# Optimization experiments

Measured on AMD Instinct MI355X. Metric: run time of the kernel, lower is better.

Reference implementation:

```python
import jax, jax.numpy as jnp
import numpy as np
from jax.scipy.special import logsumexp

L = 15      # DATA_MAX_SEG_LEN
K = 64      # XCRIBE_DIM
H = 16      # SEG_DIM
TAG = 32    # TAG_DIM
DUR = 4     # DURATION_DIM
NY = 15     # len(LABELS)
N = 16384   # sequence length
S = 2048    # number of gold segments
NEG = jnp.float32(-1e30)


def setup_inputs() -> dict:
    key = jax.random.key(0)
    ks = jax.random.split(key, 24)
    sL = 1.0 / np.sqrt(H)
    sV = 1.0 / np.sqrt(2 * H + TAG + DUR)
    sW = 1.0 / np.sqrt(H)

    def U(k, shape, s):
        return jax.random.uniform(k, shape, jnp.float32, -s, s)

    return dict(
        data=jax.random.normal(ks[0], (N, K), jnp.float32),
        fwd_Wih=U(ks[1], (4 * H, K), sL), fwd_Whh=U(ks[2], (4 * H, H), sL),
        fwd_bih=U(ks[3], (4 * H,), sL), fwd_bhh=U(ks[4], (4 * H,), sL),
        bwd_Wih=U(ks[5], (4 * H, K), sL), bwd_Whh=U(ks[6], (4 * H, H), sL),
        bwd_bih=U(ks[7], (4 * H,), sL), bwd_bhh=U(ks[8], (4 * H,), sL),
        fwd_h0=jax.random.normal(ks[9], (H,), jnp.float32),
        fwd_c0=jax.random.normal(ks[10], (H,), jnp.float32),
        bwd_h0=jax.random.normal(ks[11], (H,), jnp.float32),
        bwd_c0=jax.random.normal(ks[12], (H,), jnp.float32),
        Y_enc=jax.random.normal(ks[13], (NY, TAG), jnp.float32),
        Z_enc=jax.random.normal(ks[14], (L, DUR), jnp.float32),
        V_W=U(ks[15], (H, 2 * H + TAG + DUR), sV), V_b=U(ks[16], (H,), sV),
        W_W=U(ks[17], (1, H), sW), W_b=U(ks[18], (1,), sW),
        tags=jax.random.randint(ks[19], (S,), 0, NY),
        lengths=jax.random.randint(ks[20], (S,), 1, L + 1),
    )


def _lstm(xs, Wih, Whh, bih, bhh, h0, c0):
    # xs: [L, B, K] -> hidden outputs [L, B, H]; torch gate order i,f,g,o
    B = xs.shape[1]
    b = bih + bhh

    def step(carry, x):
        h, c = carry
        g = x @ Wih.T + h @ Whh.T + b
        i, f, gg, o = jnp.split(g, 4, axis=-1)
        c = jax.nn.sigmoid(f) * c + jax.nn.sigmoid(i) * jnp.tanh(gg)
        h = jax.nn.sigmoid(o) * jnp.tanh(c)
        return (h, c), h

    init = (jnp.broadcast_to(h0, (B, H)), jnp.broadcast_to(c0, (B, H)))
    _, hs = jax.lax.scan(step, init, xs)
    return hs


def reference(data, fwd_Wih, fwd_Whh, fwd_bih, fwd_bhh, fwd_h0, fwd_c0,
              bwd_Wih, bwd_Whh, bwd_bih, bwd_bhh, bwd_h0, bwd_c0,
              Y_enc, Z_enc, V_W, V_b, W_W, W_b, tags, lengths):
    n = data.shape[0]
    pos = jnp.arange(n)[:, None]      # [N,1]
    dd = jnp.arange(L)[None, :]       # [1,L]
    idx_f = jnp.minimum(pos + dd, n - 1)   # forward window indices
    idx_b = pos - dd                       # backward window indices (may be <0)

    win_f = data[idx_f].transpose(1, 0, 2)                  # [L,N,K]
    win_b = data[jnp.maximum(idx_b, 0)].transpose(1, 0, 2)  # [L,N,K]

    # fwd[i,d] = forward_precalc[i][i+d]; bwd[e,d] = backward_precalc[e-d][e]
    fwd = _lstm(win_f, fwd_Wih, fwd_Whh, fwd_bih, fwd_bhh, fwd_h0, fwd_c0).transpose(1, 0, 2)
    bwd = _lstm(win_b, bwd_Wih, bwd_Whh, bwd_bih, bwd_bhh, bwd_h0, bwd_c0).transpose(1, 0, 2)

    # gather fwd at (start=e-d, duration index d) -> aligned with end position e
    fwd_g = fwd[jnp.maximum(idx_b, 0), dd]          # [N,L,H]
    fb = jnp.concatenate([fwd_g, bwd], axis=-1)     # [N,L,2H]

    # split V across concat blocks: [fwd,bwd | Y | Z]
    V1 = V_W[:, :2 * H]; V2 = V_W[:, 2 * H:2 * H + TAG]; V3 = V_W[:, 2 * H + TAG:]
    base = fb @ V1.T + (Z_enc @ V3.T)[None, :, :] + V_b      # [N,L,H]
    ypart = Y_enc @ V2.T                                     # [NY,H]
    pre = base[:, :, None, :] + ypart[None, None, :, :]      # [N,L,NY,H]
    scores = jnp.tanh(pre) @ W_W[0] + W_b[0]                 # [N,L,NY]

    valid = idx_b >= 0
    A = jnp.where(valid, logsumexp(scores, axis=-1), NEG)    # [N,L] lse over labels

    # semi-Markov forward DP: log_alpha[i] = lse_d(log_alpha[i-d] + A[i-1,d-1])
    def dp(hist, a):  # hist[k] = log_alpha[i-1-k]
        new = logsumexp(hist + a)
        return jnp.concatenate([new[None], hist[:-1]]), new

    hist0 = jnp.full((L,), NEG, jnp.float32).at[0].set(0.0)
    _, alphas = jax.lax.scan(dp, hist0, A)
    logZ = alphas[-1]

    # gold-segment score; original never advances `chars`, so start is always 0
    gv = lengths < L
    gscores = scores[lengths - 1, lengths - 1, tags]
    indiv = jnp.sum(jnp.where(gv, gscores, 0.0))
    return logZ - indiv
```

## Files before the change

### kernel.cpp

```cpp
#include <hip/hip_runtime.h>

#define NPOS 16384
#define NEG  (-1e30f)

#define OFF_FWDH  0
#define OFF_BWDH  1966080
#define OFF_T0    4194304
#define OFF_R     4251904
#define OFF_IND   4255776

struct Params {
    const float *data, *fWih, *fWhh, *fbih, *fbhh, *bWih, *bWhh, *bbih, *bbhh;
    const float *h0f, *c0f, *h0b, *c0b, *Yenc, *Zenc, *VW, *Vb, *WW, *Wb;
    const int *tags, *lengths;
    float *ws; float *out;
};

typedef _Float16 half2_t __attribute__((ext_vector_type(2)));

__device__ __forceinline__ half2_t u2h(unsigned int v) {
    return __builtin_bit_cast(half2_t, v);
}
__device__ __forceinline__ unsigned int packh(float a, float b) {
    half2_t h = { (_Float16)a, (_Float16)b };
    return __builtin_bit_cast(unsigned int, h);
}
__device__ __forceinline__ float fdot2_(unsigned int w, unsigned int x, float acc) {
    return __builtin_amdgcn_fdot2(u2h(w), u2h(x), acc, false);
}
__device__ __forceinline__ float sigf(float x) {
    return __builtin_amdgcn_rcpf(1.0f + __expf(-x));
}
__device__ __forceinline__ float tanhf_(float x) {
    return 1.0f - 2.0f * __builtin_amdgcn_rcpf(1.0f + __expf(2.0f * x));
}
__device__ __forceinline__ float lse15(const float* tv) {
    float a0 = fmaxf(tv[0], tv[1]),  a1 = fmaxf(tv[2], tv[3]);
    float a2 = fmaxf(tv[4], tv[5]),  a3 = fmaxf(tv[6], tv[7]);
    float a4 = fmaxf(tv[8], tv[9]),  a5 = fmaxf(tv[10], tv[11]);
    float a6 = fmaxf(tv[12], tv[13]);
    float b0 = fmaxf(a0, a1), b1 = fmaxf(a2, a3), b2 = fmaxf(a4, a5), b3 = fmaxf(a6, tv[14]);
    float mx = fmaxf(fmaxf(b0, b1), fmaxf(b2, b3));
    float e[15];
    #pragma unroll
    for (int i = 0; i < 15; i++) e[i] = __expf(tv[i] - mx);
    float s0 = e[0]+e[1], s1 = e[2]+e[3], s2 = e[4]+e[5], s3 = e[6]+e[7];
    float s4 = e[8]+e[9], s5 = e[10]+e[11], s6 = e[12]+e[13];
    float t0 = s0+s1, t1 = s2+s3, t2 = s4+s5, t3 = s6+e[14];
    return mx + __logf((t0+t1) + (t2+t3));
}

__device__ __forceinline__ void lse_mm(const float* src, float* dst, int nprod,
                                       int tid, int nthr)
{
    const int tot = nprod * 225;
    for (int e = tid; e < tot; e += nthr) {
        const int m = e / 225;
        const int r = e - m * 225;
        const int i = r / 15;
        const int j = r - i * 15;
        const float* Ar = src + (2*m + 1)*240 + i*16;
        const float* Bc = src + (2*m)*240 + j;
        float tv[15];
        #pragma unroll
        for (int k = 0; k < 15; k++) tv[k] = Ar[k] + Bc[k*16];
        dst[m*240 + i*16 + j] = lse15(tv);
    }
}

__global__ __launch_bounds__(512) void kA(Params p)
{
    __shared__ unsigned int xs2[78*33];
    __shared__ float xgT[64*78];
    __shared__ unsigned int hsh[2*512];
    __shared__ unsigned int wqx[2048];
    __shared__ unsigned int wqh[512];
    __shared__ float bq[64];

    const int tid  = threadIdx.x;
    const int lane = tid & 63;
    const int wq   = __builtin_amdgcn_readfirstlane(tid >> 6);
    const int dir  = blockIdx.y;
    const int P0   = blockIdx.x << 6;
    const int dbase = P0 - (dir ? 14 : 0);

    const float* Wih = dir ? p.bWih : p.fWih;
    const float* Whh = dir ? p.bWhh : p.fWhh;
    const float* bih = dir ? p.bbih : p.fbih;
    const float* bhh = dir ? p.bbhh : p.fbhh;
    const float* h0  = dir ? p.h0b  : p.h0f;
    const float* c0  = dir ? p.c0b  : p.c0f;

    for (int e = tid; e < 2048; e += 512) {
        int k2 = e >> 6, pi = e & 63;
        int w = pi >> 3, jj = pi & 7;
        int j = ((jj >> 1) << 4) + 2*w + (jj & 1);
        wqx[e] = packh(Wih[j*64 + 2*k2], Wih[j*64 + 2*k2 + 1]);
    }
    if (tid < 512) {
        int m2 = tid >> 6, pi = tid & 63;
        int w = pi >> 3, jj = pi & 7;
        int j = ((jj >> 1) << 4) + 2*w + (jj & 1);
        wqh[tid] = packh(Whh[j*16 + 2*m2], Whh[j*16 + 2*m2 + 1]);
    }
    if (tid < 64) {
        int w = tid >> 3, jj = tid & 7;
        int j = ((jj >> 1) << 4) + 2*w + (jj & 1);
        bq[tid] = bih[j] + bhh[j];
    }
    for (int idx = tid; idx < 78*32; idx += 512) {
        int r = idx >> 5, c = idx & 31;
        int q = dbase + r;
        q = q < 0 ? 0 : (q > NPOS-1 ? NPOS-1 : q);
        float2 x2 = *(const float2*)(p.data + (size_t)q*64 + c*2);
        xs2[r*33 + c] = packh(x2.x, x2.y);
    }
    if (tid < 512) {
        int m2 = tid >> 6;
        hsh[tid] = packh(h0[2*m2], h0[2*m2 + 1]);
    }
    __syncthreads();

    {
        float acc[8];
        #pragma unroll
        for (int jj = 0; jj < 8; jj++) acc[jj] = bq[wq*8 + jj];
        #pragma unroll 8
        for (int k2 = 0; k2 < 32; k2++) {
            unsigned int xp = xs2[lane*33 + k2];
            uint4 w0 = *(const uint4*)&wqx[k2*64 + wq*8];
            uint4 w1 = *(const uint4*)&wqx[k2*64 + wq*8 + 4];
            acc[0] = fdot2_(w0.x, xp, acc[0]);
            acc[1] = fdot2_(w0.y, xp, acc[1]);
            acc[2] = fdot2_(w0.z, xp, acc[2]);
            acc[3] = fdot2_(w0.w, xp, acc[3]);
            acc[4] = fdot2_(w1.x, xp, acc[4]);
            acc[5] = fdot2_(w1.y, xp, acc[5]);
            acc[6] = fdot2_(w1.z, xp, acc[6]);
            acc[7] = fdot2_(w1.w, xp, acc[7]);
        }
        #pragma unroll
        for (int jj = 0; jj < 8; jj++) xgT[(wq*8 + jj)*78 + lane] = acc[jj];
    }
    #pragma unroll
    for (int it = 0; it < 2; it++) {
        int e = tid + it*512;
        if (e < 896) {
            int rw = 64 + (e >> 6);
            int g  = e & 63;
            float acc = bq[g];
            #pragma unroll 8
            for (int k2 = 0; k2 < 32; k2++)
                acc = fdot2_(wqx[k2*64 + g], xs2[rw*33 + k2], acc);
            xgT[g*78 + rw] = acc;
        }
    }
    float cv0 = c0[wq*2], cv1 = c0[wq*2 + 1];
    unsigned int* outH = (unsigned int*)(p.ws + (dir ? OFF_BWDH : OFF_FWDH));
    __syncthreads();

    int buf = 0;
    for (int d = 0; d < 15; d++) {
        const int row = dir ? (lane + 14 - d) : (lane + d);
        float part[8];
        #pragma unroll
        for (int jj = 0; jj < 8; jj++) part[jj] = xgT[(wq*8 + jj)*78 + row];
        #pragma unroll
        for (int m2 = 0; m2 < 8; m2++) {
            unsigned int hp = hsh[buf*512 + m2*64 + lane];
            uint4 w0 = *(const uint4*)&wqh[m2*64 + wq*8];
            uint4 w1 = *(const uint4*)&wqh[m2*64 + wq*8 + 4];
            part[0] = fdot2_(w0.x, hp, part[0]);
            part[1] = fdot2_(w0.y, hp, part[1]);
            part[2] = fdot2_(w0.z, hp, part[2]);
            part[3] = fdot2_(w0.w, hp, part[3]);
            part[4] = fdot2_(w1.x, hp, part[4]);
            part[5] = fdot2_(w1.y, hp, part[5]);
            part[6] = fdot2_(w1.z, hp, part[6]);
            part[7] = fdot2_(w1.w, hp, part[7]);
        }
        float cn0 = sigf(part[2])*cv0 + sigf(part[0])*tanhf_(part[4]);
        float cn1 = sigf(part[3])*cv1 + sigf(part[1])*tanhf_(part[5]);
        cv0 = cn0; cv1 = cn1;
        float h0v = sigf(part[6])*tanhf_(cn0);
        float h1v = sigf(part[7])*tanhf_(cn1);
        unsigned int pk = packh(h0v, h1v);
        hsh[(buf^1)*512 + wq*64 + lane] = pk;
        outH[((size_t)d*NPOS + P0 + lane)*8 + wq] = pk;
        __syncthreads();
        buf ^= 1;
    }
}

__global__ __launch_bounds__(1024) void kBC(Params p)
{
    __shared__ float As[64*17];
    __shared__ unsigned int VWh[256];
    __shared__ float zbl[240];
    __shared__ float EY[240];
    __shared__ float Ms[16*240];
    __shared__ float Mp[8*240];
    __shared__ float gscL[240];
    __shared__ float red[16];
    const int tid = threadIdx.x;
    const int P0  = blockIdx.x << 6;
    float* ws = p.ws;

    if (tid < 240) {
        int y = tid >> 4, h = tid & 15;
        const float4* Y4 = (const float4*)(p.Yenc + y*32);
        const float4* V4 = (const float4*)(p.VW + h*68 + 32);
        float acc = 0.f;
        #pragma unroll
        for (int t = 0; t < 8; t++) {
            float4 a = Y4[t], b = V4[t];
            acc += a.x*b.x + a.y*b.y + a.z*b.z + a.w*b.w;
        }
        EY[tid] = __expf(acc + acc);
        float4 z4 = *(const float4*)(p.Zenc + y*4);
        float4 v3 = *(const float4*)(p.VW + h*68 + 64);
        zbl[tid] = p.Vb[h] + z4.x*v3.x + z4.y*v3.y + z4.z*v3.z + z4.w*v3.w;
    }
    if (tid < 256) {
        int h = tid >> 4, j2 = tid & 15;
        int col = (j2 < 8) ? 2*j2 : 16 + 2*(j2 - 8);
        VWh[tid] = packh(p.VW[h*68 + col], p.VW[h*68 + col + 1]);
    }
    __syncthreads();

    const int pl = tid & 63;
    const int d  = tid >> 6;
    const int pp = P0 + pl;
    float Aval = NEG;
    if (d < 15 && pp >= d) {
        const uint4* fptr = (const uint4*)((const unsigned int*)(ws + OFF_FWDH)
                            + ((size_t)d*NPOS + (pp - d))*8);
        const uint4* bptr = (const uint4*)((const unsigned int*)(ws + OFF_BWDH)
                            + ((size_t)d*NPOS + pp)*8);
        uint4 f0 = fptr[0], f1 = fptr[1];
        uint4 b0 = bptr[0], b1 = bptr[1];
        unsigned int fp_[8] = {f0.x, f0.y, f0.z, f0.w, f1.x, f1.y, f1.z, f1.w};
        unsigned int bp_[8] = {b0.x, b0.y, b0.z, b0.w, b1.x, b1.y, b1.z, b1.w};
        float E[16], w2[16], wsum = 0.f;
        #pragma unroll
        for (int h = 0; h < 16; h++) {
            float acc = zbl[d*16 + h];
            uint4 va = *(const uint4*)&VWh[h*16];
            uint4 vb = *(const uint4*)&VWh[h*16 + 4];
            uint4 vc = *(const uint4*)&VWh[h*16 + 8];
            uint4 vd = *(const uint4*)&VWh[h*16 + 12];
            acc = fdot2_(va.x, fp_[0], acc); acc = fdot2_(va.y, fp_[1], acc);
            acc = fdot2_(va.z, fp_[2], acc); acc = fdot2_(va.w, fp_[3], acc);
            acc = fdot2_(vb.x, fp_[4], acc); acc = fdot2_(vb.y, fp_[5], acc);
            acc = fdot2_(vb.z, fp_[6], acc); acc = fdot2_(vb.w, fp_[7], acc);
            acc = fdot2_(vc.x, bp_[0], acc); acc = fdot2_(vc.y, bp_[1], acc);
            acc = fdot2_(vc.z, bp_[2], acc); acc = fdot2_(vc.w, bp_[3], acc);
            acc = fdot2_(vd.x, bp_[4], acc); acc = fdot2_(vd.y, bp_[5], acc);
            acc = fdot2_(vd.z, bp_[6], acc); acc = fdot2_(vd.w, bp_[7], acc);
            E[h] = __expf(acc + acc);
            float w = p.WW[h];
            w2[h] = -2.0f * w;
            wsum += w;
        }
        const float cst = p.Wb[0] + wsum;
        float sc[15];
        #pragma unroll
        for (int y = 0; y < 15; y++) {
            float a = 0.f;
            #pragma unroll
            for (int h = 0; h < 16; h++)
                a = fmaf(w2[h], __builtin_amdgcn_rcpf(1.0f + E[h]*EY[y*16 + h]), a);
            sc[y] = cst + a;
        }
        Aval = lse15(sc);
        if (pp == d && pp < 15) {
            #pragma unroll
            for (int y = 0; y < 15; y++) gscL[pp*16 + y] = sc[y];
        }
    }
    As[pl*17 + d] = Aval;
    __syncthreads();

    {
        const int wv = tid >> 6;
        const int ln = tid & 63;
        if (ln < 15) {
            float s[15];
            #pragma unroll
            for (int i = 0; i < 15; i++) s[i] = (i == ln) ? 0.f : NEG;
            const int t0 = wv * 4;
            #pragma unroll
            for (int q = 0; q < 4; q++) {
                const int t = t0 + q;
                float tv[15];
                #pragma unroll
                for (int i = 0; i < 15; i++) tv[i] = s[i] + As[t*17 + i];
                float nw = lse15(tv);
                #pragma unroll
                for (int i = 14; i > 0; i--) s[i] = s[i-1];
                s[0] = nw;
            }
            #pragma unroll
            for (int i = 0; i < 15; i++) Ms[wv*240 + i*16 + ln] = s[i];
        }
    }
    __syncthreads();

    lse_mm(Ms, Mp, 8, tid, 1024);  __syncthreads();
    lse_mm(Mp, Ms, 4, tid, 1024);  __syncthreads();
    lse_mm(Ms, Mp, 2, tid, 1024);  __syncthreads();
    if (tid < 225) {
        const int i = tid / 15, j = tid - (tid / 15) * 15;
        float tv[15];
        #pragma unroll
        for (int k = 0; k < 15; k++) tv[k] = Mp[240 + i*16 + k] + Mp[k*16 + j];
        (ws + OFF_T0)[blockIdx.x*225 + i*15 + j] = lse15(tv);
    }

    if (blockIdx.x == 0) {
        float loc = 0.f;
        for (int s = tid; s < 2048; s += 1024) {
            int len = p.lengths[s];
            if (len < 15) loc += gscL[(len-1)*16 + p.tags[s]];
        }
        #pragma unroll
        for (int off = 32; off > 0; off >>= 1) loc += __shfl_down(loc, off);
        if ((tid & 63) == 0) red[tid >> 6] = loc;
        __syncthreads();
        if (tid == 0) {
            float ind = 0.f;
            #pragma unroll
            for (int q = 0; q < 16; q++) ind += red[q];
            ws[OFF_IND] = ind;
        }
    }
}

__global__ __launch_bounds__(1024) void kD(Params p)
{
    __shared__ float Ms[16*240];
    __shared__ float Mp[8*240];
    const int tid = threadIdx.x;
    const int g   = blockIdx.x;
    const float* T0 = p.ws + OFF_T0;

    for (int idx = tid; idx < 16*225; idx += 1024) {
        int t = idx / 225, r = idx - t*225;
        Ms[t*240 + (r/15)*16 + (r%15)] = T0[((g<<4) + t)*225 + r];
    }
    __syncthreads();
    lse_mm(Ms, Mp, 8, tid, 1024); __syncthreads();
    lse_mm(Mp, Ms, 4, tid, 1024); __syncthreads();
    lse_mm(Ms, Mp, 2, tid, 1024); __syncthreads();
    if (tid < 225) {
        const int i = tid / 15, j = tid - (tid / 15) * 15;
        float tv[15];
        #pragma unroll
        for (int k = 0; k < 15; k++) tv[k] = Mp[240 + i*16 + k] + Mp[k*16 + j];
        p.ws[OFF_R + g*225 + i*15 + j] = lse15(tv);
    }
}

__global__ __launch_bounds__(1024) void kE(Params p)
{
    __shared__ float Ms[16*240];
    __shared__ float Mp[8*240];
    const int tid = threadIdx.x;
    const float* Rg = p.ws + OFF_R;

    for (int idx = tid; idx < 16*225; idx += 1024) {
        int t = idx / 225, r = idx - t*225;
        Ms[t*240 + (r/15)*16 + (r%15)] = Rg[t*225 + r];
    }
    __syncthreads();
    lse_mm(Ms, Mp, 8, tid, 1024); __syncthreads();
    lse_mm(Mp, Ms, 4, tid, 1024); __syncthreads();
    lse_mm(Ms, Mp, 2, tid, 1024); __syncthreads();
    if (tid == 0) {
        float tv[15];
        #pragma unroll
        for (int k = 0; k < 15; k++) tv[k] = Mp[240 + k] + Mp[k*16];
        float logZ = lse15(tv);
        p.out[0] = logZ - p.ws[OFF_IND];
    }
}

extern "C" void kernel_launch(void* const* d_in, const int* in_sizes, int n_in,
                              void* d_out, int out_size, void* d_ws, size_t ws_size,
                              hipStream_t stream)
{
    Params prm;
    prm.data = (const float*)d_in[0];
    prm.fWih = (const float*)d_in[1];
    prm.fWhh = (const float*)d_in[2];
    prm.fbih = (const float*)d_in[3];
    prm.fbhh = (const float*)d_in[4];
    prm.bWih = (const float*)d_in[5];
    prm.bWhh = (const float*)d_in[6];
    prm.bbih = (const float*)d_in[7];
    prm.bbhh = (const float*)d_in[8];
    prm.h0f  = (const float*)d_in[9];
    prm.c0f  = (const float*)d_in[10];
    prm.h0b  = (const float*)d_in[11];
    prm.c0b  = (const float*)d_in[12];
    prm.Yenc = (const float*)d_in[13];
    prm.Zenc = (const float*)d_in[14];
    prm.VW   = (const float*)d_in[15];
    prm.Vb   = (const float*)d_in[16];
    prm.WW   = (const float*)d_in[17];
    prm.Wb   = (const float*)d_in[18];
    prm.tags    = (const int*)d_in[19];
    prm.lengths = (const int*)d_in[20];
    prm.ws  = (float*)d_ws;
    prm.out = (float*)d_out;

    hipLaunchKernelGGL(kA,  dim3(256, 2), dim3(512),  0, stream, prm);
    hipLaunchKernelGGL(kBC, dim3(256),    dim3(1024), 0, stream, prm);
    hipLaunchKernelGGL(kD,  dim3(16),     dim3(1024), 0, stream, prm);
    hipLaunchKernelGGL(kE,  dim3(1),      dim3(1024), 0, stream, prm);
}
```

Baseline: 163.6 us.

## Transpose LSTM hidden layout and merge DP reduction kernels into one

New measurement: 214.9 us. 1.31x slower.

```diff
diff --git a/kernel.cpp b/kernel.cpp
--- a/kernel.cpp
+++ b/kernel.cpp
@@ -186,7 +186,7 @@
         float h1v = sigf(part[7])*tanhf_(cn1);
         unsigned int pk = packh(h0v, h1v);
         hsh[(buf^1)*512 + wq*64 + lane] = pk;
-        outH[((size_t)d*NPOS + P0 + lane)*8 + wq] = pk;
+        outH[(size_t)(d*8 + wq)*NPOS + P0 + lane] = pk;
         __syncthreads();
         buf ^= 1;
     }
@@ -233,14 +233,14 @@
     const int pp = P0 + pl;
     float Aval = NEG;
     if (d < 15 && pp >= d) {
-        const uint4* fptr = (const uint4*)((const unsigned int*)(ws + OFF_FWDH)
-                            + ((size_t)d*NPOS + (pp - d))*8);
-        const uint4* bptr = (const uint4*)((const unsigned int*)(ws + OFF_BWDH)
-                            + ((size_t)d*NPOS + pp)*8);
-        uint4 f0 = fptr[0], f1 = fptr[1];
-        uint4 b0 = bptr[0], b1 = bptr[1];
-        unsigned int fp_[8] = {f0.x, f0.y, f0.z, f0.w, f1.x, f1.y, f1.z, f1.w};
-        unsigned int bp_[8] = {b0.x, b0.y, b0.z, b0.w, b1.x, b1.y, b1.z, b1.w};
+        const unsigned int* fH = (const unsigned int*)(ws + OFF_FWDH);
+        const unsigned int* bH = (const unsigned int*)(ws + OFF_BWDH);
+        unsigned int fp_[8], bp_[8];
+        #pragma unroll
+        for (int w = 0; w < 8; w++) {
+            fp_[w] = fH[(size_t)(d*8 + w)*NPOS + (pp - d)];
+            bp_[w] = bH[(size_t)(d*8 + w)*NPOS + pp];
+        }
         float E[16], w2[16], wsum = 0.f;
         #pragma unroll
         for (int h = 0; h < 16; h++) {
@@ -336,46 +336,35 @@
     }
 }
 
-__global__ __launch_bounds__(1024) void kD(Params p)
+__global__ __launch_bounds__(1024) void kF(Params p)
 {
-    __shared__ float Ms[16*240];
-    __shared__ float Mp[8*240];
+    __shared__ float Ms[64*240];
+    __shared__ float Mp[32*240];
+    __shared__ float Gs[4*240];
     const int tid = threadIdx.x;
-    const int g   = blockIdx.x;
     const float* T0 = p.ws + OFF_T0;
 
-    for (int idx = tid; idx < 16*225; idx += 1024) {
-        int t = idx / 225, r = idx - t*225;
-        Ms[t*240 + (r/15)*16 + (r%15)] = T0[((g<<4) + t)*225 + r];
-    }
-    __syncthreads();
-    lse_mm(Ms, Mp, 8, tid, 1024); __syncthreads();
-    lse_mm(Mp, Ms, 4, tid, 1024); __syncthreads();
-    lse_mm(Ms, Mp, 2, tid, 1024); __syncthreads();
-    if (tid < 225) {
-        const int i = tid / 15, j = tid - (tid / 15) * 15;
-        float tv[15];
-        #pragma unroll
-        for (int k = 0; k < 15; k++) tv[k] = Mp[240 + i*16 + k] + Mp[k*16 + j];
-        p.ws[OFF_R + g*225 + i*15 + j] = lse15(tv);
-    }
-}
-
-__global__ __launch_bounds__(1024) void kE(Params p)
-{
-    __shared__ float Ms[16*240];
-    __shared__ float Mp[8*240];
-    const int tid = threadIdx.x;
-    const float* Rg = p.ws + OFF_R;
-
-    for (int idx = tid; idx < 16*225; idx += 1024) {
-        int t = idx / 225, r = idx - t*225;
-        Ms[t*240 + (r/15)*16 + (r%15)] = Rg[t*225 + r];
-    }
-    __syncthreads();
-    lse_mm(Ms, Mp, 8, tid, 1024); __syncthreads();
-    lse_mm(Mp, Ms, 4, tid, 1024); __syncthreads();
-    lse_mm(Ms, Mp, 2, tid, 1024); __syncthreads();
+    for (int c = 0; c < 4; c++) {
+        for (int idx = tid; idx < 64*225; idx += 1024) {
+            int t = idx / 225, r = idx - t*225;
+            Ms[t*240 + (r/15)*16 + (r%15)] = T0[(c*64 + t)*225 + r];
+        }
+        __syncthreads();
+        lse_mm(Ms, Mp, 32, tid, 1024); __syncthreads();
+        lse_mm(Mp, Ms, 16, tid, 1024); __syncthreads();
+        lse_mm(Ms, Mp,  8, tid, 1024); __syncthreads();
+        lse_mm(Mp, Ms,  4, tid, 1024); __syncthreads();
+        lse_mm(Ms, Mp,  2, tid, 1024); __syncthreads();
+        if (tid < 225) {
+            const int i = tid / 15, j = tid - (tid / 15) * 15;
+            float tv[15];
+            #pragma unroll
+            for (int k = 0; k < 15; k++) tv[k] = Mp[240 + i*16 + k] + Mp[k*16 + j];
+            Gs[c*240 + i*16 + j] = lse15(tv);
+        }
+        __syncthreads();
+    }
+    lse_mm(Gs, Mp, 2, tid, 1024); __syncthreads();
     if (tid == 0) {
         float tv[15];
         #pragma unroll
@@ -416,6 +405,5 @@
 
     hipLaunchKernelGGL(kA,  dim3(256, 2), dim3(512),  0, stream, prm);
     hipLaunchKernelGGL(kBC, dim3(256),    dim3(1024), 0, stream, prm);
-    hipLaunchKernelGGL(kD,  dim3(16),     dim3(1024), 0, stream, prm);
-    hipLaunchKernelGGL(kE,  dim3(1),      dim3(1024), 0, stream, prm);
-}
+    hipLaunchKernelGGL(kF,  dim3(1),      dim3(1024), 0, stream, prm);
+}
```
